# Kernel tuning notes

Measured on AMD Instinct MI355X. Metric: run time of the kernel, lower is better.

The kernel has to match this reference:

```python
import jax, jax.numpy as jnp
import numpy as np
import math

B, C, H, W, S = 8, 512, 64, 64, 4


def setup_inputs() -> dict:
    key = jax.random.key(0)
    ks = jax.random.split(key, 7)
    s = 1.0 / math.sqrt(C)  # ~ torch Linear init scale
    x = jax.random.normal(ks[0], (B, C, H, W), jnp.float32)
    Wq = jax.random.uniform(ks[1], (C, C), jnp.float32, -s, s)
    bq = jax.random.uniform(ks[2], (C,), jnp.float32, -s, s)
    Wk = jax.random.uniform(ks[3], (C, C), jnp.float32, -s, s)
    bk = jax.random.uniform(ks[4], (C,), jnp.float32, -s, s)
    Wv = jax.random.uniform(ks[5], (C, C), jnp.float32, -s, s)
    bv = jax.random.uniform(ks[6], (C,), jnp.float32, -s, s)
    return {"x": x, "Wq": Wq, "bq": bq, "Wk": Wk, "bk": bk, "Wv": Wv, "bv": bv}


def reference(x, Wq, bq, Wk, bk, Wv, bv):
    # x: (B, C, H, W). Faithful to the torch module's output, but expressed
    # in the algebraically-equivalent efficient form: the repeat_interleaved
    # attention matrix A is block-constant, so out = repeat(A_m @ Vsum).
    b, c, h, w = x.shape
    nb = (h // S) * (w // S)  # number of SxS spatial blocks
    hw = h * w
    ss = S * S

    # Block means in unfold order (bh, bw): (B, nb, C)
    x_avg = x.reshape(b, c, h // S, S, w // S, S).mean(axis=(3, 5))
    x_avg = x_avg.reshape(b, c, nb).transpose(0, 2, 1)

    Q = x_avg @ Wq.T + bq  # (B, nb, C)
    K = x_avg @ Wk.T + bk  # (B, nb, C)
    A = jax.nn.softmax(jnp.einsum('bnc,bmc->bnm', Q, K) / jnp.sqrt(jnp.float32(c)), axis=-1)

    # V over flat row-major pixels: (B, HW, C)
    x_flat = x.reshape(b, c, hw).transpose(0, 2, 1)
    V = x_flat @ Wv.T + bv

    # repeat_interleave on dim=2 means column group j of A sums V rows
    # [j*ss, (j+1)*ss) in FLAT pixel order (not spatial blocks) - faithful.
    Vsum = V.reshape(b, hw // ss, ss, c).sum(axis=2)  # (B, nb, C)
    out_small = jnp.einsum('bnm,bmc->bnc', A, Vsum)   # (B, nb, C)
    # repeat_interleave on dim=1: each block row broadcast to ss flat pixels
    out_flat = jnp.repeat(out_small, ss, axis=1)      # (B, HW, C)
    return out_flat.transpose(0, 2, 1).reshape(b, c, h, w)
```

## Files before the change

### kernel.cpp

```cpp
#include <hip/hip_runtime.h>

typedef __attribute__((ext_vector_type(8))) short short8;
typedef __attribute__((ext_vector_type(4))) float f32x4;

__device__ __forceinline__ unsigned short f2bf(float f) {
    union { float f; unsigned int i; } v; v.f = f;
    unsigned int x = v.i;
    return (unsigned short)((x + 0x7FFFu + ((x >> 16) & 1u)) >> 16);
}
__device__ __forceinline__ f32x4 mfma16(short8 a, short8 b, f32x4 c) {
    return __builtin_amdgcn_mfma_f32_16x16x32_bf16(a, b, c, 0, 0, 0);
}

__global__ void prep_kernel(const float* __restrict__ x,
                            const float* __restrict__ Wq,
                            const float* __restrict__ Wk,
                            const float* __restrict__ Wv,
                            unsigned short* __restrict__ xavg,
                            unsigned short* __restrict__ xsum,
                            unsigned short* __restrict__ Wb)
{
    const int blk = blockIdx.x;
    const int t = threadIdx.x;
    if (blk >= 4096) {
        const int f = (blk - 4096) * 512 + t;
        const int m = f >> 16;
        const int o = f & 65535;
        const float4* s4 = (const float4*)((m == 0) ? Wq : (m == 1) ? Wk : Wv);
        float4 a = s4[o];
        float4 b = s4[o + 256];
        ushort4* d4 = (ushort4*)(Wb + (size_t)m * 262144);
        d4[o]       = make_ushort4(f2bf(a.x), f2bf(a.y), f2bf(a.z), f2bf(a.w));
        d4[o + 256] = make_ushort4(f2bf(b.x), f2bf(b.y), f2bf(b.z), f2bf(b.w));
        return;
    }
    const int b = blk >> 9;
    const int c = blk & 511;

    const float4* x4 = (const float4*)(x + (size_t)blk * 4096);
    float4 f0 = x4[t], f1 = x4[t + 256], f2 = x4[t + 512], f3 = x4[t + 768];

    __shared__ float part2[1024];
    part2[t]       = f0.x + f0.y + f0.z + f0.w;
    part2[t + 256] = f1.x + f1.y + f1.z + f1.w;
    part2[t + 512] = f2.x + f2.y + f2.z + f2.w;
    part2[t + 768] = f3.x + f3.y + f3.z + f3.w;
    __syncthreads();

    {
        const int base = 16 * (t >> 2) + 4 * (t & 3);
        float4 q = *(const float4*)&part2[base];
        xsum[((size_t)b * 256 + t) * 512 + c] = f2bf(q.x + q.y + q.z + q.w);
    }
    {
        const int bh = t >> 4, bw = t & 15;
        float m = (part2[(bh * 4 + 0) * 16 + bw] + part2[(bh * 4 + 1) * 16 + bw] +
                   part2[(bh * 4 + 2) * 16 + bw] + part2[(bh * 4 + 3) * 16 + bw]) * 0.0625f;
        xavg[((size_t)b * 256 + t) * 512 + c] = f2bf(m);
    }
}

__global__ void __launch_bounds__(256, 2)
proj_gemm(const unsigned short* __restrict__ xavg,
          const unsigned short* __restrict__ xsum,
          const unsigned short* __restrict__ Wb,
          const float* __restrict__ bq,
          const float* __restrict__ bk,
          const float* __restrict__ bv,
          unsigned short* __restrict__ QK,
          unsigned short* __restrict__ VsT)
{
    const int blk = blockIdx.x;
    const int lane = threadIdx.x & 63, quad = lane >> 4, r16 = lane & 15;
    const int w = threadIdx.x >> 6;

    if (blk < 256) {
        const int wave = blk * 4 + w;
        const int mt2 = wave >> 4;
        const int nt4 = wave & 15;
        const unsigned short* xp0 = xavg + (size_t)(mt2 * 32 + r16) * 512 + quad * 8;
        const unsigned short* xp1 = xp0 + 16 * 512;
        const unsigned short* wp0 = Wb + (size_t)(nt4 * 64 + r16) * 512 + quad * 8;
        const unsigned short* wp1 = wp0 + 16 * 512;
        const unsigned short* wp2 = wp0 + 32 * 512;
        const unsigned short* wp3 = wp0 + 48 * 512;

        f32x4 a00 = {0,0,0,0}, a01 = a00, a02 = a00, a03 = a00;
        f32x4 a10 = a00, a11 = a00, a12 = a00, a13 = a00;
#pragma unroll 4
        for (int k = 0; k < 512; k += 32) {
            short8 qa0 = *(const short8*)(xp0 + k);
            short8 qa1 = *(const short8*)(xp1 + k);
            short8 b0 = *(const short8*)(wp0 + k);
            short8 b1 = *(const short8*)(wp1 + k);
            short8 b2 = *(const short8*)(wp2 + k);
            short8 b3 = *(const short8*)(wp3 + k);
            a00 = mfma16(qa0, b0, a00); a01 = mfma16(qa0, b1, a01);
            a02 = mfma16(qa0, b2, a02); a03 = mfma16(qa0, b3, a03);
            a10 = mfma16(qa1, b0, a10); a11 = mfma16(qa1, b1, a11);
            a12 = mfma16(qa1, b2, a12); a13 = mfma16(qa1, b3, a13);
        }
        const int row0 = mt2 * 32 + quad * 4;
        f32x4 accs0[4] = {a00, a01, a02, a03};
        f32x4 accs1[4] = {a10, a11, a12, a13};
#pragma unroll
        for (int j = 0; j < 4; ++j) {
            const int c = nt4 * 64 + j * 16 + r16;
            const float bias = (c < 512) ? bq[c] : bk[c - 512];
#pragma unroll
            for (int r = 0; r < 4; ++r) {
                QK[(size_t)(row0 + r) * 1024 + c]      = f2bf(accs0[j][r] + bias);
                QK[(size_t)(row0 + 16 + r) * 1024 + c] = f2bf(accs1[j][r] + bias);
            }
        }
    } else {
        const int vblk = blk - 256;
        const int b = vblk >> 4;
        const int wave = (vblk & 15) * 4 + w;
        const int mt2 = wave >> 3;
        const int nt4 = wave & 7;
        const unsigned short* xp0 = xsum + (size_t)b * 131072 + (size_t)(mt2 * 32 + r16) * 512 + quad * 8;
        const unsigned short* xp1 = xp0 + 16 * 512;
        const unsigned short* wp0 = Wb + 524288 + (size_t)(nt4 * 64 + r16) * 512 + quad * 8;
        const unsigned short* wp1 = wp0 + 16 * 512;
        const unsigned short* wp2 = wp0 + 32 * 512;
        const unsigned short* wp3 = wp0 + 48 * 512;

        f32x4 a00 = {0,0,0,0}, a01 = a00, a02 = a00, a03 = a00;
        f32x4 a10 = a00, a11 = a00, a12 = a00, a13 = a00;
#pragma unroll 4
        for (int k = 0; k < 512; k += 32) {
            short8 qa0 = *(const short8*)(xp0 + k);
            short8 qa1 = *(const short8*)(xp1 + k);
            short8 b0 = *(const short8*)(wp0 + k);
            short8 b1 = *(const short8*)(wp1 + k);
            short8 b2 = *(const short8*)(wp2 + k);
            short8 b3 = *(const short8*)(wp3 + k);
            a00 = mfma16(qa0, b0, a00); a01 = mfma16(qa0, b1, a01);
            a02 = mfma16(qa0, b2, a02); a03 = mfma16(qa0, b3, a03);
            a10 = mfma16(qa1, b0, a10); a11 = mfma16(qa1, b1, a11);
            a12 = mfma16(qa1, b2, a12); a13 = mfma16(qa1, b3, a13);
        }
        unsigned short* vb = VsT + (size_t)b * 131072;
        const int m0 = mt2 * 32 + quad * 4;
        f32x4 accs0[4] = {a00, a01, a02, a03};
        f32x4 accs1[4] = {a10, a11, a12, a13};
#pragma unroll
        for (int j = 0; j < 4; ++j) {
            const int c = nt4 * 64 + j * 16 + r16;
            const float bias = 16.f * bv[c];
#pragma unroll
            for (int r = 0; r < 4; ++r) {
                vb[(size_t)c * 256 + m0 + r]      = f2bf(accs0[j][r] + bias);
                vb[(size_t)c * 256 + m0 + 16 + r] = f2bf(accs1[j][r] + bias);
            }
        }
    }
}

__global__ void __launch_bounds__(256, 2)
score_av(const unsigned short* __restrict__ QK,
         const unsigned short* __restrict__ VsT,
         float* __restrict__ out)
{
    __shared__ union {
        float S[16][257];
        float osT[256][17];
    } u;
    __shared__ __align__(16) unsigned short Abf[16][264];

    const int b = blockIdx.y;
    const int strip = blockIdx.x >> 1;
    const int chalf = blockIdx.x & 1;
    const int w = threadIdx.x >> 6, lane = threadIdx.x & 63;
    const int quad = lane >> 4, r16 = lane & 15;

    {
        const unsigned short* qp = QK + (size_t)(b * 256 + strip * 16 + r16) * 1024 + quad * 8;
        const unsigned short* kp0 = QK + (size_t)(b * 256 + w * 64 + r16) * 1024 + 512 + quad * 8;
        const unsigned short* kp1 = kp0 + 16 * 1024;
        const unsigned short* kp2 = kp0 + 32 * 1024;
        const unsigned short* kp3 = kp0 + 48 * 1024;

        f32x4 a0 = {0,0,0,0}, a1 = a0, a2 = a0, a3 = a0;
#pragma unroll 4
        for (int k = 0; k < 512; k += 32) {
            short8 qa = *(const short8*)(qp + k);
            short8 b0 = *(const short8*)(kp0 + k);
            short8 b1 = *(const short8*)(kp1 + k);
            short8 b2 = *(const short8*)(kp2 + k);
            short8 b3 = *(const short8*)(kp3 + k);
            a0 = mfma16(qa, b0, a0); a1 = mfma16(qa, b1, a1);
            a2 = mfma16(qa, b2, a2); a3 = mfma16(qa, b3, a3);
        }
        f32x4 accs[4] = {a0, a1, a2, a3};
#pragma unroll
        for (int j = 0; j < 4; ++j) {
            const int col = w * 64 + j * 16 + r16;
#pragma unroll
            for (int r = 0; r < 4; ++r)
                u.S[quad * 4 + r][col] = accs[j][r];
        }
    }
    __syncthreads();

    {
        const int t = threadIdx.x;
        const int r = t >> 4, idx = t & 15;
        float v[16];
        float mx = -3.4e38f;
#pragma unroll
        for (int j = 0; j < 16; ++j) {
            v[j] = u.S[r][idx * 16 + j] * 0.044194173824159216f;
            mx = fmaxf(mx, v[j]);
        }
        mx = fmaxf(mx, __shfl_xor(mx, 1));
        mx = fmaxf(mx, __shfl_xor(mx, 2));
        mx = fmaxf(mx, __shfl_xor(mx, 4));
        mx = fmaxf(mx, __shfl_xor(mx, 8));
        float sum = 0.f;
#pragma unroll
        for (int j = 0; j < 16; ++j) { v[j] = __expf(v[j] - mx); sum += v[j]; }
        sum += __shfl_xor(sum, 1);
        sum += __shfl_xor(sum, 2);
        sum += __shfl_xor(sum, 4);
        sum += __shfl_xor(sum, 8);
        const float inv = 1.f / sum;
        unsigned short* ap = &Abf[r][idx * 16];
#pragma unroll
        for (int j = 0; j < 16; j += 4)
            *(ushort4*)(ap + j) = make_ushort4(f2bf(v[j] * inv), f2bf(v[j + 1] * inv),
                                               f2bf(v[j + 2] * inv), f2bf(v[j + 3] * inv));
    }
    __syncthreads();

    {
        f32x4 acc0 = {0,0,0,0}, acc1 = acc0, acc2 = acc0, acc3 = acc0;
        const unsigned short* vbase = VsT + (size_t)b * 131072 +
                                      (size_t)(chalf * 256 + w * 64 + r16) * 256 + quad * 8;
        const unsigned short* vp0 = vbase;
        const unsigned short* vp1 = vbase + 16 * 256;
        const unsigned short* vp2 = vbase + 32 * 256;
        const unsigned short* vp3 = vbase + 48 * 256;
#pragma unroll
        for (int kk = 0; kk < 256; kk += 32) {
            short8 a = *(const short8*)(&Abf[r16][kk + quad * 8]);
            short8 b0 = *(const short8*)(vp0 + kk);
            short8 b1 = *(const short8*)(vp1 + kk);
            short8 b2 = *(const short8*)(vp2 + kk);
            short8 b3 = *(const short8*)(vp3 + kk);
            acc0 = mfma16(a, b0, acc0); acc1 = mfma16(a, b1, acc1);
            acc2 = mfma16(a, b2, acc2); acc3 = mfma16(a, b3, acc3);
        }
        __syncthreads();
        f32x4 accs[4] = {acc0, acc1, acc2, acc3};
#pragma unroll
        for (int i = 0; i < 4; ++i) {
            const int cl = w * 64 + i * 16 + r16;
#pragma unroll
            for (int r = 0; r < 4; ++r)
                u.osT[cl][quad * 4 + r] = accs[i][r];
        }
    }
    __syncthreads();

    {
        const int t = threadIdx.x;
        const float* orow = &u.osT[t][0];
        float* obase = out + (size_t)(b * 512 + chalf * 256 + t) * 4096 + strip * 256;
#pragma unroll
        for (int n = 0; n < 16; ++n) {
            const float v = orow[n];
            float4 v4 = make_float4(v, v, v, v);
            *(float4*)(obase + n * 16)      = v4;
            *(float4*)(obase + n * 16 + 4)  = v4;
            *(float4*)(obase + n * 16 + 8)  = v4;
            *(float4*)(obase + n * 16 + 12) = v4;
        }
    }
}

extern "C" void kernel_launch(void* const* d_in, const int* in_sizes, int n_in,
                              void* d_out, int out_size, void* d_ws, size_t ws_size,
                              hipStream_t stream) {
    const float* x  = (const float*)d_in[0];
    const float* Wq = (const float*)d_in[1];
    const float* bq = (const float*)d_in[2];
    const float* Wk = (const float*)d_in[3];
    const float* bk = (const float*)d_in[4];
    const float* Wv = (const float*)d_in[5];
    const float* bv = (const float*)d_in[6];
    float* out = (float*)d_out;

    unsigned short* Wb   = (unsigned short*)d_ws;
    unsigned short* xavg = Wb + 786432;
    unsigned short* xsum = xavg + 1048576;
    unsigned short* QK   = xsum + 1048576;
    unsigned short* VsT  = QK + 2097152;

    prep_kernel<<<4480, 256, 0, stream>>>(x, Wq, Wk, Wv, xavg, xsum, Wb);
    proj_gemm<<<384, 256, 0, stream>>>(xavg, xsum, Wb, bq, bk, bv, QK, VsT);
    score_av<<<dim3(32, 8), 256, 0, stream>>>(QK, VsT, out);
}
```

Before: 185.0 us.

## Shrink projection GEMM wave tiles to 32x32 and coalesce output broadcast stores

The projection GEMM now gives each wave a 32x32 output tile instead of 32x64 and launches twice as many blocks, with the occupancy hint raised to 3 blocks per CU. This adds parallelism and spreads the work over more CUs, at the cost of reloading each A fragment for more tiles. The score_av epilogue is also rewritten so that 64 lanes write consecutive float4s along a channel row, replacing per-thread strided row writes, to improve coalescing of the large broadcast output store.

```diff
diff --git a/kernel.cpp b/kernel.cpp
--- a/kernel.cpp
+++ b/kernel.cpp
@@ -60,7 +60,7 @@
     }
 }
 
-__global__ void __launch_bounds__(256, 2)
+__global__ void __launch_bounds__(256, 3)
 proj_gemm(const unsigned short* __restrict__ xavg,
           const unsigned short* __restrict__ xsum,
           const unsigned short* __restrict__ Wb,
@@ -74,38 +74,31 @@
     const int lane = threadIdx.x & 63, quad = lane >> 4, r16 = lane & 15;
     const int w = threadIdx.x >> 6;
 
-    if (blk < 256) {
+    if (blk < 512) {
         const int wave = blk * 4 + w;
-        const int mt2 = wave >> 4;
-        const int nt4 = wave & 15;
-        const unsigned short* xp0 = xavg + (size_t)(mt2 * 32 + r16) * 512 + quad * 8;
+        const int mt = wave >> 5;
+        const int nt = wave & 31;
+        const unsigned short* xp0 = xavg + (size_t)(mt * 32 + r16) * 512 + quad * 8;
         const unsigned short* xp1 = xp0 + 16 * 512;
-        const unsigned short* wp0 = Wb + (size_t)(nt4 * 64 + r16) * 512 + quad * 8;
+        const unsigned short* wp0 = Wb + (size_t)(nt * 32 + r16) * 512 + quad * 8;
         const unsigned short* wp1 = wp0 + 16 * 512;
-        const unsigned short* wp2 = wp0 + 32 * 512;
-        const unsigned short* wp3 = wp0 + 48 * 512;
-
-        f32x4 a00 = {0,0,0,0}, a01 = a00, a02 = a00, a03 = a00;
-        f32x4 a10 = a00, a11 = a00, a12 = a00, a13 = a00;
+
+        f32x4 a00 = {0,0,0,0}, a01 = a00, a10 = a00, a11 = a00;
 #pragma unroll 4
         for (int k = 0; k < 512; k += 32) {
             short8 qa0 = *(const short8*)(xp0 + k);
             short8 qa1 = *(const short8*)(xp1 + k);
             short8 b0 = *(const short8*)(wp0 + k);
             short8 b1 = *(const short8*)(wp1 + k);
-            short8 b2 = *(const short8*)(wp2 + k);
-            short8 b3 = *(const short8*)(wp3 + k);
             a00 = mfma16(qa0, b0, a00); a01 = mfma16(qa0, b1, a01);
-            a02 = mfma16(qa0, b2, a02); a03 = mfma16(qa0, b3, a03);
             a10 = mfma16(qa1, b0, a10); a11 = mfma16(qa1, b1, a11);
-            a12 = mfma16(qa1, b2, a12); a13 = mfma16(qa1, b3, a13);
-        }
-        const int row0 = mt2 * 32 + quad * 4;
-        f32x4 accs0[4] = {a00, a01, a02, a03};
-        f32x4 accs1[4] = {a10, a11, a12, a13};
-#pragma unroll
-        for (int j = 0; j < 4; ++j) {
-            const int c = nt4 * 64 + j * 16 + r16;
+        }
+        const int row0 = mt * 32 + quad * 4;
+        f32x4 accs0[2] = {a00, a01};
+        f32x4 accs1[2] = {a10, a11};
+#pragma unroll
+        for (int j = 0; j < 2; ++j) {
+            const int c = nt * 32 + j * 16 + r16;
             const float bias = (c < 512) ? bq[c] : bk[c - 512];
 #pragma unroll
             for (int r = 0; r < 4; ++r) {
@@ -114,40 +107,33 @@
             }
         }
     } else {
-        const int vblk = blk - 256;
-        const int b = vblk >> 4;
-        const int wave = (vblk & 15) * 4 + w;
-        const int mt2 = wave >> 3;
-        const int nt4 = wave & 7;
+        const int vblk = blk - 512;
+        const int b = vblk >> 5;
+        const int wib = (vblk & 31) * 4 + w;
+        const int mt2 = wib >> 4;
+        const int nt = wib & 15;
         const unsigned short* xp0 = xsum + (size_t)b * 131072 + (size_t)(mt2 * 32 + r16) * 512 + quad * 8;
         const unsigned short* xp1 = xp0 + 16 * 512;
-        const unsigned short* wp0 = Wb + 524288 + (size_t)(nt4 * 64 + r16) * 512 + quad * 8;
+        const unsigned short* wp0 = Wb + 524288 + (size_t)(nt * 32 + r16) * 512 + quad * 8;
         const unsigned short* wp1 = wp0 + 16 * 512;
-        const unsigned short* wp2 = wp0 + 32 * 512;
-        const unsigned short* wp3 = wp0 + 48 * 512;
-
-        f32x4 a00 = {0,0,0,0}, a01 = a00, a02 = a00, a03 = a00;
-        f32x4 a10 = a00, a11 = a00, a12 = a00, a13 = a00;
+
+        f32x4 a00 = {0,0,0,0}, a01 = a00, a10 = a00, a11 = a00;
 #pragma unroll 4
         for (int k = 0; k < 512; k += 32) {
             short8 qa0 = *(const short8*)(xp0 + k);
             short8 qa1 = *(const short8*)(xp1 + k);
             short8 b0 = *(const short8*)(wp0 + k);
             short8 b1 = *(const short8*)(wp1 + k);
-            short8 b2 = *(const short8*)(wp2 + k);
-            short8 b3 = *(const short8*)(wp3 + k);
             a00 = mfma16(qa0, b0, a00); a01 = mfma16(qa0, b1, a01);
-            a02 = mfma16(qa0, b2, a02); a03 = mfma16(qa0, b3, a03);
             a10 = mfma16(qa1, b0, a10); a11 = mfma16(qa1, b1, a11);
-            a12 = mfma16(qa1, b2, a12); a13 = mfma16(qa1, b3, a13);
         }
         unsigned short* vb = VsT + (size_t)b * 131072;
         const int m0 = mt2 * 32 + quad * 4;
-        f32x4 accs0[4] = {a00, a01, a02, a03};
-        f32x4 accs1[4] = {a10, a11, a12, a13};
-#pragma unroll
-        for (int j = 0; j < 4; ++j) {
-            const int c = nt4 * 64 + j * 16 + r16;
+        f32x4 accs0[2] = {a00, a01};
+        f32x4 accs1[2] = {a10, a11};
+#pragma unroll
+        for (int j = 0; j < 2; ++j) {
+            const int c = nt * 32 + j * 16 + r16;
             const float bias = 16.f * bv[c];
 #pragma unroll
             for (int r = 0; r < 4; ++r) {
@@ -265,17 +251,13 @@
     __syncthreads();
 
     {
-        const int t = threadIdx.x;
-        const float* orow = &u.osT[t][0];
-        float* obase = out + (size_t)(b * 512 + chalf * 256 + t) * 4096 + strip * 256;
-#pragma unroll
-        for (int n = 0; n < 16; ++n) {
-            const float v = orow[n];
-            float4 v4 = make_float4(v, v, v, v);
-            *(float4*)(obase + n * 16)      = v4;
-            *(float4*)(obase + n * 16 + 4)  = v4;
-            *(float4*)(obase + n * 16 + 8)  = v4;
-            *(float4*)(obase + n * 16 + 12) = v4;
+        const int j = threadIdx.x & 63;
+        float* obase = out + (size_t)(b * 512 + chalf * 256) * 4096 + strip * 256 + j * 4;
+#pragma unroll
+        for (int it = 0; it < 64; ++it) {
+            const int ch = it * 4 + w;
+            const float v = u.osT[ch][j >> 2];
+            *(float4*)(obase + (size_t)ch * 4096) = make_float4(v, v, v, v);
         }
     }
 }
@@ -299,6 +281,6 @@
     unsigned short* VsT  = QK + 2097152;
 
     prep_kernel<<<4480, 256, 0, stream>>>(x, Wq, Wk, Wv, xavg, xsum, Wb);
-    proj_gemm<<<384, 256, 0, stream>>>(xavg, xsum, Wb, bq, bk, bv, QK, VsT);
+    proj_gemm<<<768, 256, 0, stream>>>(xavg, xsum, Wb, bq, bk, bv, QK, VsT);
     score_av<<<dim3(32, 8), 256, 0, stream>>>(QK, VsT, out);
 }
```

New measurement: 172.5 us. 1.07x faster.
